# Kernel optimization log

Measured on AMD Instinct MI355X. Metric: run time of the kernel, lower is better.

## Reference

```python
import jax, jax.numpy as jnp
import numpy as np

D = 768      # hidden_size
H = 12       # num_head
HD = D // H  # head_dim
LN_EPS = 1e-5


def setup_inputs() -> dict:
    key = jax.random.key(0)
    ks = jax.random.split(key, 9)
    N, S = 4, 2048
    s = 0.02
    return {
        "hidden_state": jax.random.normal(ks[0], (N, S, D), dtype=jnp.float32),
        "key_padding_mask": jax.random.randint(ks[1], (N, S), 0, 2, dtype=jnp.int64),
        "Wq": jax.random.normal(ks[2], (D, D), dtype=jnp.float32) * s,
        "Wk": jax.random.normal(ks[3], (D, D), dtype=jnp.float32) * s,
        "Wv": jax.random.normal(ks[4], (D, D), dtype=jnp.float32) * s,
        "Wo": jax.random.normal(ks[5], (D, D), dtype=jnp.float32) * s,
        "W1": jax.random.normal(ks[6], (4 * D, D), dtype=jnp.float32) * s,
        "W2": jax.random.normal(ks[7], (D, 4 * D), dtype=jnp.float32) * s,
        "ln_g": jnp.ones((D,), dtype=jnp.float32),
        "ln_b": jnp.zeros((D,), dtype=jnp.float32),
    }


def _layernorm(x, g, b):
    mu = jnp.mean(x, axis=-1, keepdims=True)
    var = jnp.mean(jnp.square(x - mu), axis=-1, keepdims=True)
    return (x - mu) * jax.lax.rsqrt(var + LN_EPS) * g + b


def reference(hidden_state, key_padding_mask, Wq, Wk, Wv, Wo, W1, W2, ln_g, ln_b):
    x = hidden_state
    N, S, _ = x.shape
    # Note: original module projects K and V from `query` (self-attention).
    def proj(W):
        return (x @ W.T).reshape(N, S, H, HD).transpose(0, 2, 1, 3)  # [N,H,S,HD]
    Q, K, V = proj(Wq), proj(Wk), proj(Wv)
    scores = jnp.einsum("bhqd,bhkd->bhqk", Q, K)  # [N,H,S,S]
    # int mask: 0 marks padding positions -> masked with -inf
    pad = (key_padding_mask == 0)[:, None, None, :]  # [N,1,1,S]
    scores = jnp.where(pad, -jnp.inf, scores)
    attn = jax.nn.softmax(scores / np.sqrt(HD), axis=-1)
    ctx = jnp.einsum("bhqk,bhkd->bhqd", attn, V)
    ctx = ctx.transpose(0, 2, 1, 3).reshape(N, S, D)
    mha = ctx @ Wo.T
    # residual + LayerNorm (same LN params used twice, as in the original)
    n1 = _layernorm(x + mha, ln_g, ln_b)
    # FFN with exact GELU (torch nn.GELU default)
    f = jax.nn.gelu(n1 @ W1.T, approximate=False) @ W2.T
    return _layernorm(n1 + f, ln_g, ln_b)
```

## Files before the change

kernel.cpp:

```cpp
#include <hip/hip_runtime.h>
#include <math.h>

typedef unsigned short u16;
typedef unsigned int u32;
typedef __bf16 bf16x8 __attribute__((ext_vector_type(8)));
typedef float f32x4 __attribute__((ext_vector_type(4)));
typedef u32 u32x4 __attribute__((ext_vector_type(4)));

#define NB 4
#define SS 2048
#define DD 768
#define HH 12
#define HD 64
#define ROWS (NB*SS)

__device__ __forceinline__ u16 f2bf(float f) {
    union { float f; unsigned u; } v; v.f = f;
    unsigned r = v.u + 0x7fffu + ((v.u >> 16) & 1u);
    return (u16)(r >> 16);
}
__device__ __forceinline__ u32 fas(float f) { union { float f; u32 u; } v; v.f = f; return v.u; }

__device__ __forceinline__ void gl_lds16(const void* g, void* l) {
    __builtin_amdgcn_global_load_lds((__attribute__((address_space(1))) void*)(g),
                                     (__attribute__((address_space(3))) void*)(l),
                                     16, 0, 0);
}

__global__ __launch_bounds__(256) void prep_kernel(
        const float* __restrict__ X, const float* __restrict__ Wq,
        const float* __restrict__ Wk, const float* __restrict__ Wv,
        const float* __restrict__ Wo, const float* __restrict__ W1,
        const float* __restrict__ W2, const int* __restrict__ mask,
        u16* __restrict__ Xb, u16* __restrict__ Wqkvb, u16* __restrict__ Wob,
        u16* __restrict__ W1b, u16* __restrict__ W2b,
        int* __restrict__ cidx, int* __restrict__ cnt) {
    const int blk = blockIdx.x, tid = threadIdx.x;
    const float* src; u16* dst; int idx;
    if (blk < 6144)       { src = X;  dst = Xb;               idx = blk * 1024 + tid * 4; }
    else if (blk < 6720)  { src = Wq; dst = Wqkvb;            idx = (blk - 6144) * 1024 + tid * 4; }
    else if (blk < 7296)  { src = Wk; dst = Wqkvb + DD * DD;  idx = (blk - 6720) * 1024 + tid * 4; }
    else if (blk < 7872)  { src = Wv; dst = Wqkvb + 2*DD*DD;  idx = (blk - 7296) * 1024 + tid * 4; }
    else if (blk < 8448)  { src = Wo; dst = Wob;              idx = (blk - 7872) * 1024 + tid * 4; }
    else if (blk < 10752) { src = W1; dst = W1b;              idx = (blk - 8448) * 1024 + tid * 4; }
    else if (blk < 13056) { src = W2; dst = W2b;              idx = (blk - 10752) * 1024 + tid * 4; }
    else {
        const int b = blk - 13056;
        const int lane = tid & 63, wave = tid >> 6;
        const int base = b * SS + tid * 8;
        int4 m0 = *(const int4*)&mask[base];
        int4 m1 = *(const int4*)&mask[base + 4];
        int v[8] = { m0.x != 0, m0.y != 0, m0.z != 0, m0.w != 0,
                     m1.x != 0, m1.y != 0, m1.z != 0, m1.w != 0 };
        int own = 0;
#pragma unroll
        for (int i = 0; i < 8; ++i) own += v[i];
        int inc = own;
#pragma unroll
        for (int o = 1; o < 64; o <<= 1) {
            int n = __shfl_up(inc, o);
            if (lane >= o) inc += n;
        }
        __shared__ int wsum[4];
        if (lane == 63) wsum[wave] = inc;
        __syncthreads();
        int wbase = 0;
#pragma unroll
        for (int w = 0; w < 4; ++w) wbase += (w < wave) ? wsum[w] : 0;
        int pos = wbase + inc - own;
        int o8[8];
#pragma unroll
        for (int i = 0; i < 8; ++i) { o8[i] = v[i] ? pos : -1; pos += v[i]; }
        *(int4*)&cidx[base]     = make_int4(o8[0], o8[1], o8[2], o8[3]);
        *(int4*)&cidx[base + 4] = make_int4(o8[4], o8[5], o8[6], o8[7]);
        if (tid == 255) cnt[b] = wbase + inc;
        return;
    }
    float4 v = *(const float4*)&src[idx];
    ushort4 o;
    o.x = f2bf(v.x); o.y = f2bf(v.y); o.z = f2bf(v.z); o.w = f2bf(v.w);
    *(ushort4*)&dst[idx] = o;
}

template <int EPI, int BN, int BK>
__global__ __launch_bounds__(256) void gemm_bt(const u16* __restrict__ A,
                                               const u16* __restrict__ B,
                                               int M, int N, int K,
                                               void* __restrict__ out,
                                               const void* __restrict__ aux,
                                               u16* __restrict__ Qb,
                                               u16* __restrict__ Kb,
                                               u16* __restrict__ Vb,
                                               const int* __restrict__ cidx) {
    constexpr int NH = BK / 64;
    __shared__ __align__(16) u16 lA[NH][128 * 64];
    __shared__ __align__(16) u16 lB[NH][BN * 64];
    constexpr int MI = (BN == 128) ? 4 : 2;
    const int tid = threadIdx.x;
    const int lane = tid & 63, wave = tid >> 6;
    const int quad = lane >> 4, lc = lane & 15;
    const int xcd = blockIdx.x & 7, loc = blockIdx.x >> 3;
    const int mb = xcd * 8 + (loc & 7), nb = loc >> 3;
    const int m0 = mb * 128, n0 = nb * BN;
    const int wrow = (BN == 128) ? (wave >> 1) * 64 : wave * 32;
    const int wcol = (BN == 128) ? (wave & 1) * 64 : 0;
    const int swz = lc & 7;

    f32x4 acc[MI][4] = {};

    for (int kb = 0; kb < K; kb += BK) {
        __syncthreads();
#pragma unroll
        for (int h = 0; h < NH; ++h) {
#pragma unroll
            for (int p0 = 0; p0 < 1024; p0 += 256) {
                int p = p0 + tid, row = p >> 3, cl = (p & 7) ^ (row & 7);
                gl_lds16(A + (size_t)(m0 + row) * K + kb + h * 64 + cl * 8,
                         &lA[h][(size_t)(p0 + wave * 64) * 8]);
            }
#pragma unroll
            for (int p0 = 0; p0 < BN * 8; p0 += 256) {
                int p = p0 + tid, row = p >> 3, cl = (p & 7) ^ (row & 7);
                gl_lds16(B + (size_t)(n0 + row) * K + kb + h * 64 + cl * 8,
                         &lB[h][(size_t)(p0 + wave * 64) * 8]);
            }
        }
        __syncthreads();
#pragma unroll
        for (int h = 0; h < NH; ++h)
#pragma unroll
            for (int k2 = 0; k2 < 2; ++k2) {
                bf16x8 af[MI], bfr[4];
#pragma unroll
                for (int t = 0; t < MI; ++t)
                    af[t] = *(const bf16x8*)&lA[h][(wrow + t * 16 + lc) * 64 + ((quad + k2 * 4) ^ swz) * 8];
#pragma unroll
                for (int t = 0; t < 4; ++t)
                    bfr[t] = *(const bf16x8*)&lB[h][(wcol + t * 16 + lc) * 64 + ((quad + k2 * 4) ^ swz) * 8];
#pragma unroll
                for (int mi = 0; mi < MI; ++mi)
#pragma unroll
                    for (int ni = 0; ni < 4; ++ni)
                        acc[mi][ni] = __builtin_amdgcn_mfma_f32_16x16x32_bf16(af[mi], bfr[ni],
                                                                             acc[mi][ni], 0, 0, 0);
            }
    }

#pragma unroll
    for (int mi = 0; mi < MI; ++mi) {
        int csa[4];
        if constexpr (EPI == 0) {
            int mbase = m0 + wrow + mi * 16 + quad * 4;
            int4 cs4 = *(const int4*)&cidx[(mbase >> 11) * SS + (mbase & 2047)];
            csa[0] = cs4.x; csa[1] = cs4.y; csa[2] = cs4.z; csa[3] = cs4.w;
        }
#pragma unroll
        for (int r = 0; r < 4; ++r) {
            int m = m0 + wrow + mi * 16 + quad * 4 + r;
#pragma unroll
            for (int ni = 0; ni < 4; ++ni) {
                int n = n0 + wcol + ni * 16 + lc;
                float v = acc[mi][ni][r];
                if constexpr (EPI == 0) {
                    int b = m >> 11, s = m & 2047;
                    int which = n / DD, rem = n - which * DD;
                    int h = rem >> 6, d = rem & 63;
                    u16* dst = which == 0 ? Qb : (which == 1 ? Kb : Vb);
                    int sidx = which == 0 ? s : csa[r];
                    if (sidx >= 0)
                        dst[((((size_t)b * HH + h) * SS + sidx) << 6) + d] = f2bf(v);
                } else if constexpr (EPI == 1) {
                    float u = v * fmaf(v * v, 0.035677408f, 0.7978845608f);
                    float e = __builtin_amdgcn_exp2f(u * 2.885390082f);
                    float g = v - v * __builtin_amdgcn_rcpf(e + 1.0f);
                    ((u16*)out)[(size_t)m * N + n] = f2bf(g);
                } else if constexpr (EPI == 2) {
                    ((float*)out)[(size_t)m * N + n] =
                        v + ((const float*)aux)[(size_t)m * N + n];
                } else {
                    ((float*)out)[(size_t)m * N + n] =
                        v + (float)(((const __bf16*)aux)[(size_t)m * N + n]);
                }
            }
        }
    }
}

__global__ __launch_bounds__(256) void transpose_v(const u16* __restrict__ V,
                                                   u16* __restrict__ Vt,
                                                   const int* __restrict__ cnt) {
    __shared__ u16 t[32][33];
    int bh = blockIdx.z;
    int c = cnt[bh / HH];
    int cr = (c + 63) & ~63;
    int s0 = blockIdx.x * 32, d0 = blockIdx.y * 32;
    if (s0 >= cr) return;
    const u16* vb = V + (size_t)bh * SS * HD;
    u16* vtb = Vt + (size_t)bh * HD * SS;
    int tx = threadIdx.x & 31, ty = threadIdx.x >> 5;
#pragma unroll
    for (int i = 0; i < 32; i += 8) {
        int s = s0 + ty + i;
        t[ty + i][tx] = (s < c) ? vb[(size_t)s * HD + d0 + tx] : (u16)0;
    }
    __syncthreads();
#pragma unroll
    for (int i = 0; i < 32; i += 8) vtb[(size_t)(d0 + ty + i) * SS + s0 + tx] = t[tx][ty + i];
}

__global__ __launch_bounds__(256, 3) void attn_kernel(const u16* __restrict__ Q,
                                                      const u16* __restrict__ K,
                                                      const u16* __restrict__ Vt,
                                                      const int* __restrict__ cntg,
                                                      u16* __restrict__ Ctx) {
    __shared__ __align__(16) u16 lK[2][4096];
    __shared__ __align__(16) u16 lV[2][4096];
    const int tid = threadIdx.x, lane = tid & 63, wave = tid >> 6;
    const int quad = lane >> 4, lc = lane & 15;
    const int bh = blockIdx.x % (NB * HH);
    const int b = bh / HH, h = bh - b * HH;
    const int q0 = (blockIdx.x / (NB * HH)) * 128;
    const u16* Qg = Q + ((size_t)bh * SS + q0 + wave * 32) * HD;
    const u16* Kg = K + (size_t)bh * SS * HD;
    const u16* Vg = Vt + (size_t)bh * HD * SS;
    const int sw = lc & 7;
    const int cnt = cntg[b];
    const int nt = (cnt + 63) >> 6;

    const int srow = tid >> 3, scl = (tid & 7) ^ (srow & 7);
    const int srow2 = (256 + tid) >> 3, scl2 = (tid & 7) ^ (srow2 & 7);

    auto stage = [&](int bi, int j0) {
        gl_lds16(Kg + (size_t)(j0 + srow) * HD + scl * 8,   &lK[bi][(size_t)(wave * 64) * 8]);
        gl_lds16(Kg + (size_t)(j0 + srow2) * HD + scl2 * 8, &lK[bi][(size_t)(256 + wave * 64) * 8]);
        gl_lds16(Vg + (size_t)srow * SS + j0 + scl * 8,     &lV[bi][(size_t)(wave * 64) * 8]);
        gl_lds16(Vg + (size_t)srow2 * SS + j0 + scl2 * 8,   &lV[bi][(size_t)(256 + wave * 64) * 8]);
    };

    bf16x8 qf[2][2];
#pragma unroll
    for (int mi = 0; mi < 2; ++mi)
#pragma unroll
        for (int k2 = 0; k2 < 2; ++k2)
            qf[mi][k2] = *(const bf16x8*)(Qg + (size_t)(mi * 16 + lc) * HD + k2 * 32 + quad * 8);

    bf16x8 onesf;
#pragma unroll
    for (int i = 0; i < 8; ++i) onesf[i] = (__bf16)1.0f;

    f32x4 oacc[2][4] = {};
    f32x4 lsum[2] = {};

    stage(0, 0);
    for (int t = 0; t < nt; ++t) {
        const int cur = t & 1;
        if (t < nt - 1) {
            stage(cur ^ 1, (t + 1) * 64);
            __builtin_amdgcn_sched_barrier(0);
            asm volatile("s_waitcnt vmcnt(4)" ::: "memory");
        } else {
            __builtin_amdgcn_sched_barrier(0);
            asm volatile("s_waitcnt vmcnt(0)" ::: "memory");
        }
        __builtin_amdgcn_sched_barrier(0);
        __builtin_amdgcn_s_barrier();
        __builtin_amdgcn_sched_barrier(0);

        const u16* bK = &lK[cur][0];
        const u16* bV = &lV[cur][0];

        f32x4 sacc[2][4] = {};
        __builtin_amdgcn_s_setprio(1);
#pragma unroll
        for (int k2 = 0; k2 < 2; ++k2) {
            bf16x8 kf[4];
#pragma unroll
            for (int ni = 0; ni < 4; ++ni)
                kf[ni] = *(const bf16x8*)&bK[(ni * 16 + lc) * 64 + ((quad + k2 * 4) ^ sw) * 8];
#pragma unroll
            for (int ni = 0; ni < 4; ++ni) {
                sacc[0][ni] = __builtin_amdgcn_mfma_f32_16x16x32_bf16(kf[ni], qf[0][k2], sacc[0][ni], 0, 0, 0);
                sacc[1][ni] = __builtin_amdgcn_mfma_f32_16x16x32_bf16(kf[ni], qf[1][k2], sacc[1][ni], 0, 0, 0);
            }
        }
        __builtin_amdgcn_s_setprio(0);

        const int kb_ = cnt - t * 64;
        const bool part = kb_ < 64;
        u32 pa[2][4], pb[2][4];
#pragma unroll
        for (int ni = 0; ni < 4; ++ni) {
#pragma unroll
            for (int mi = 0; mi < 2; ++mi) {
#pragma unroll
                for (int r = 0; r < 4; ++r) {
                    float e = __builtin_amdgcn_exp2f(sacc[mi][ni][r] * 0.180336880f);
                    if (part) e = (ni * 16 + quad * 4 + r < kb_) ? e : 0.0f;
                    sacc[mi][ni][r] = e;
                }
                pa[mi][ni] = __builtin_amdgcn_perm(fas(sacc[mi][ni][1]), fas(sacc[mi][ni][0]), 0x07060302);
                pb[mi][ni] = __builtin_amdgcn_perm(fas(sacc[mi][ni][3]), fas(sacc[mi][ni][2]), 0x07060302);
            }
        }

        bf16x8 pf[2][2];
#pragma unroll
        for (int mi = 0; mi < 2; ++mi)
#pragma unroll
            for (int k2 = 0; k2 < 2; ++k2) {
                u32 xa = pa[mi][2 * k2], ya = pa[mi][2 * k2 + 1];
                u32 xb = pb[mi][2 * k2], yb = pb[mi][2 * k2 + 1];
                asm("v_permlane32_swap_b32 %0, %1" : "+v"(xa), "+v"(ya));
                asm("v_permlane16_swap_b32 %0, %1" : "+v"(xa), "+v"(ya));
                asm("v_permlane32_swap_b32 %0, %1" : "+v"(xb), "+v"(yb));
                asm("v_permlane16_swap_b32 %0, %1" : "+v"(xb), "+v"(yb));
                u32x4 pw = { xa, xb, ya, yb };
                pf[mi][k2] = __builtin_bit_cast(bf16x8, pw);
            }

        __builtin_amdgcn_s_setprio(1);
#pragma unroll
        for (int k2 = 0; k2 < 2; ++k2) {
            lsum[0] = __builtin_amdgcn_mfma_f32_16x16x32_bf16(pf[0][k2], onesf, lsum[0], 0, 0, 0);
            lsum[1] = __builtin_amdgcn_mfma_f32_16x16x32_bf16(pf[1][k2], onesf, lsum[1], 0, 0, 0);
#pragma unroll
            for (int ni = 0; ni < 4; ++ni) {
                bf16x8 vf = *(const bf16x8*)&bV[(ni * 16 + lc) * 64 + ((quad + k2 * 4) ^ sw) * 8];
                oacc[0][ni] = __builtin_amdgcn_mfma_f32_16x16x32_bf16(pf[0][k2], vf, oacc[0][ni], 0, 0, 0);
                oacc[1][ni] = __builtin_amdgcn_mfma_f32_16x16x32_bf16(pf[1][k2], vf, oacc[1][ni], 0, 0, 0);
            }
        }
        __builtin_amdgcn_s_setprio(0);

        __builtin_amdgcn_sched_barrier(0);
        __builtin_amdgcn_s_barrier();
    }

#pragma unroll
    for (int mi = 0; mi < 2; ++mi)
#pragma unroll
        for (int r = 0; r < 4; ++r) {
            float inv = 1.0f / lsum[mi][r];
            int s = q0 + wave * 32 + mi * 16 + quad * 4 + r;
            size_t base = ((size_t)(b * SS + s)) * DD + h * HD;
#pragma unroll
            for (int ni = 0; ni < 4; ++ni)
                Ctx[base + ni * 16 + lc] = f2bf(oacc[mi][ni][r] * inv);
        }
}

__global__ __launch_bounds__(256) void ln_kernel(const float* __restrict__ in,
                                                 const float* __restrict__ g,
                                                 const float* __restrict__ bb,
                                                 u16* __restrict__ out_bf,
                                                 float* __restrict__ out_f) {
    const int row = blockIdx.x, tid = threadIdx.x;
    const float* x = in + (size_t)row * DD;
    float v0 = x[tid], v1 = x[tid + 256], v2 = x[tid + 512];
    float s = v0 + v1 + v2;
    float q = v0 * v0 + v1 * v1 + v2 * v2;
#pragma unroll
    for (int o = 1; o < 64; o <<= 1) {
        s += __shfl_xor(s, o);
        q += __shfl_xor(q, o);
    }
    __shared__ float rs[4], rq[4];
    int wave = tid >> 6;
    if ((tid & 63) == 0) { rs[wave] = s; rq[wave] = q; }
    __syncthreads();
    s = rs[0] + rs[1] + rs[2] + rs[3];
    q = rq[0] + rq[1] + rq[2] + rq[3];
    float mu = s * (1.0f / DD);
    float var = q * (1.0f / DD) - mu * mu;
    float rstd = rsqrtf(var + 1e-5f);
#pragma unroll
    for (int j = 0; j < 3; ++j) {
        int col = tid + j * 256;
        float v = (j == 0 ? v0 : (j == 1 ? v1 : v2));
        float y = (v - mu) * rstd * g[col] + bb[col];
        if (out_bf) out_bf[(size_t)row * DD + col] = f2bf(y);
        if (out_f) out_f[(size_t)row * DD + col] = y;
    }
}

extern "C" void kernel_launch(void* const* d_in, const int* in_sizes, int n_in,
                              void* d_out, int out_size, void* d_ws, size_t ws_size,
                              hipStream_t stream) {
    const float* X    = (const float*)d_in[0];
    const int*   mask = (const int*)d_in[1];
    const float* Wq   = (const float*)d_in[2];
    const float* Wk   = (const float*)d_in[3];
    const float* Wv   = (const float*)d_in[4];
    const float* Wo   = (const float*)d_in[5];
    const float* W1   = (const float*)d_in[6];
    const float* W2   = (const float*)d_in[7];
    const float* ln_g = (const float*)d_in[8];
    const float* ln_b = (const float*)d_in[9];
    float* out = (float*)d_out;

    char* ws = (char*)d_ws;
    size_t off = 0;
    auto alloc = [&](size_t bytes) {
        void* p = ws + off;
        off += (bytes + 255) & ~(size_t)255;
        return p;
    };
    u16*   Xbf   = (u16*)alloc((size_t)ROWS * DD * 2);
    u16*   Wqkvb = (u16*)alloc((size_t)3 * DD * DD * 2);
    u16*   Wob   = (u16*)alloc((size_t)DD * DD * 2);
    u16*   W1b   = (u16*)alloc((size_t)4 * DD * DD * 2);
    u16*   W2b   = (u16*)alloc((size_t)4 * DD * DD * 2);
    int*   cidx  = (int*)alloc((size_t)NB * SS * 4);
    int*   cnt   = (int*)alloc(256);
    u16*   Qb    = (u16*)alloc((size_t)ROWS * DD * 2);
    u16*   Kb    = (u16*)alloc((size_t)ROWS * DD * 2);
    u16*   Vb    = (u16*)alloc((size_t)ROWS * DD * 2);
    u16*   Vtb   = (u16*)alloc((size_t)ROWS * DD * 2);
    float* resid = (float*)alloc((size_t)ROWS * DD * 4);
    u16*   n1b   = (u16*)alloc((size_t)ROWS * DD * 2);
    u16*   Gb    = Qb;
    u16*   Ctxb  = Xbf;
    float* h2    = resid;

    prep_kernel<<<dim3(13056 + NB), dim3(256), 0, stream>>>(
        X, Wq, Wk, Wv, Wo, W1, W2, mask,
        Xbf, Wqkvb, Wob, W1b, W2b, cidx, cnt);

    gemm_bt<0, 128, 64><<<dim3((3 * DD / 128) * (ROWS / 128)), dim3(256), 0, stream>>>(
        Xbf, Wqkvb, ROWS, 3 * DD, DD, nullptr, nullptr, Qb, Kb, Vb, cidx);

    transpose_v<<<dim3(SS / 32, HD / 32, NB * HH), dim3(256), 0, stream>>>(Vb, Vtb, cnt);

    attn_kernel<<<dim3((SS / 128) * (NB * HH)), dim3(256), 0, stream>>>(
        Qb, Kb, Vtb, cnt, Ctxb);

    gemm_bt<2, 64, 128><<<dim3((DD / 64) * (ROWS / 128)), dim3(256), 0, stream>>>(
        Ctxb, Wob, ROWS, DD, DD, resid, X, nullptr, nullptr, nullptr, nullptr);

    ln_kernel<<<dim3(ROWS), dim3(256), 0, stream>>>(resid, ln_g, ln_b, n1b, nullptr);

    gemm_bt<1, 128, 64><<<dim3((4 * DD / 128) * (ROWS / 128)), dim3(256), 0, stream>>>(
        n1b, W1b, ROWS, 4 * DD, DD, Gb, nullptr, nullptr, nullptr, nullptr, nullptr);

    gemm_bt<3, 64, 128><<<dim3((DD / 64) * (ROWS / 128)), dim3(256), 0, stream>>>(
        Gb, W2b, ROWS, DD, 4 * DD, h2, n1b, nullptr, nullptr, nullptr, nullptr);

    ln_kernel<<<dim3(ROWS), dim3(256), 0, stream>>>(h2, ln_g, ln_b, nullptr, out);
}
```

Measured before the change: 333.9 us.

## Use 256-row GEMM tiles with 512 threads and one-wave-per-row LayerNorm

The GEMM template gains a BM parameter. The QKV and FFN1 GEMMs now run 256x128 tiles with 8 waves, so each B tile is loaded once for twice as many rows, and the XCD-aware block mapping is generalised to match. LayerNorm now handles one row per wavefront with 12 values per lane, which removes the shared-memory reduction and the block barrier. In exchange, the larger tiles use more LDS per block and halve the number of blocks in those GEMMs, which may hurt occupancy and load balance.

```diff
diff --git a/kernel.cpp b/kernel.cpp
--- a/kernel.cpp
+++ b/kernel.cpp
@@ -82,26 +82,28 @@
     *(ushort4*)&dst[idx] = o;
 }
 
-template <int EPI, int BN, int BK>
-__global__ __launch_bounds__(256) void gemm_bt(const u16* __restrict__ A,
-                                               const u16* __restrict__ B,
-                                               int M, int N, int K,
-                                               void* __restrict__ out,
-                                               const void* __restrict__ aux,
-                                               u16* __restrict__ Qb,
-                                               u16* __restrict__ Kb,
-                                               u16* __restrict__ Vb,
-                                               const int* __restrict__ cidx) {
+template <int EPI, int BN, int BK, int BM>
+__global__ __launch_bounds__(BM * 2) void gemm_bt(const u16* __restrict__ A,
+                                                  const u16* __restrict__ B,
+                                                  int M, int N, int K,
+                                                  void* __restrict__ out,
+                                                  const void* __restrict__ aux,
+                                                  u16* __restrict__ Qb,
+                                                  u16* __restrict__ Kb,
+                                                  u16* __restrict__ Vb,
+                                                  const int* __restrict__ cidx) {
     constexpr int NH = BK / 64;
-    __shared__ __align__(16) u16 lA[NH][128 * 64];
+    constexpr int NT = BM * 2;
+    constexpr int MPX = (ROWS / BM) / 8;
+    __shared__ __align__(16) u16 lA[NH][BM * 64];
     __shared__ __align__(16) u16 lB[NH][BN * 64];
     constexpr int MI = (BN == 128) ? 4 : 2;
     const int tid = threadIdx.x;
     const int lane = tid & 63, wave = tid >> 6;
     const int quad = lane >> 4, lc = lane & 15;
     const int xcd = blockIdx.x & 7, loc = blockIdx.x >> 3;
-    const int mb = xcd * 8 + (loc & 7), nb = loc >> 3;
-    const int m0 = mb * 128, n0 = nb * BN;
+    const int mb = xcd * MPX + (loc % MPX), nb = loc / MPX;
+    const int m0 = mb * BM, n0 = nb * BN;
     const int wrow = (BN == 128) ? (wave >> 1) * 64 : wave * 32;
     const int wcol = (BN == 128) ? (wave & 1) * 64 : 0;
     const int swz = lc & 7;
@@ -113,13 +115,13 @@
 #pragma unroll
         for (int h = 0; h < NH; ++h) {
 #pragma unroll
-            for (int p0 = 0; p0 < 1024; p0 += 256) {
+            for (int p0 = 0; p0 < BM * 8; p0 += NT) {
                 int p = p0 + tid, row = p >> 3, cl = (p & 7) ^ (row & 7);
                 gl_lds16(A + (size_t)(m0 + row) * K + kb + h * 64 + cl * 8,
                          &lA[h][(size_t)(p0 + wave * 64) * 8]);
             }
 #pragma unroll
-            for (int p0 = 0; p0 < BN * 8; p0 += 256) {
+            for (int p0 = 0; p0 < BN * 8; p0 += NT) {
                 int p = p0 + tid, row = p >> 3, cl = (p & 7) ^ (row & 7);
                 gl_lds16(B + (size_t)(n0 + row) * K + kb + h * 64 + cl * 8,
                          &lB[h][(size_t)(p0 + wave * 64) * 8]);
@@ -354,30 +356,29 @@
                                                  const float* __restrict__ bb,
                                                  u16* __restrict__ out_bf,
                                                  float* __restrict__ out_f) {
-    const int row = blockIdx.x, tid = threadIdx.x;
+    const int row = blockIdx.x * 4 + (threadIdx.x >> 6);
+    const int lane = threadIdx.x & 63;
     const float* x = in + (size_t)row * DD;
-    float v0 = x[tid], v1 = x[tid + 256], v2 = x[tid + 512];
-    float s = v0 + v1 + v2;
-    float q = v0 * v0 + v1 * v1 + v2 * v2;
+    float v[12];
+    float s = 0.0f, q = 0.0f;
+#pragma unroll
+    for (int i = 0; i < 12; ++i) {
+        v[i] = x[i * 64 + lane];
+        s += v[i];
+        q += v[i] * v[i];
+    }
 #pragma unroll
     for (int o = 1; o < 64; o <<= 1) {
         s += __shfl_xor(s, o);
         q += __shfl_xor(q, o);
     }
-    __shared__ float rs[4], rq[4];
-    int wave = tid >> 6;
-    if ((tid & 63) == 0) { rs[wave] = s; rq[wave] = q; }
-    __syncthreads();
-    s = rs[0] + rs[1] + rs[2] + rs[3];
-    q = rq[0] + rq[1] + rq[2] + rq[3];
     float mu = s * (1.0f / DD);
     float var = q * (1.0f / DD) - mu * mu;
     float rstd = rsqrtf(var + 1e-5f);
 #pragma unroll
-    for (int j = 0; j < 3; ++j) {
-        int col = tid + j * 256;
-        float v = (j == 0 ? v0 : (j == 1 ? v1 : v2));
-        float y = (v - mu) * rstd * g[col] + bb[col];
+    for (int i = 0; i < 12; ++i) {
+        int col = i * 64 + lane;
+        float y = (v[i] - mu) * rstd * g[col] + bb[col];
         if (out_bf) out_bf[(size_t)row * DD + col] = f2bf(y);
         if (out_f) out_f[(size_t)row * DD + col] = y;
     }
@@ -426,7 +427,7 @@
         X, Wq, Wk, Wv, Wo, W1, W2, mask,
         Xbf, Wqkvb, Wob, W1b, W2b, cidx, cnt);
 
-    gemm_bt<0, 128, 64><<<dim3((3 * DD / 128) * (ROWS / 128)), dim3(256), 0, stream>>>(
+    gemm_bt<0, 128, 64, 256><<<dim3((3 * DD / 128) * (ROWS / 256)), dim3(512), 0, stream>>>(
         Xbf, Wqkvb, ROWS, 3 * DD, DD, nullptr, nullptr, Qb, Kb, Vb, cidx);
 
     transpose_v<<<dim3(SS / 32, HD / 32, NB * HH), dim3(256), 0, stream>>>(Vb, Vtb, cnt);
@@ -434,16 +435,16 @@
     attn_kernel<<<dim3((SS / 128) * (NB * HH)), dim3(256), 0, stream>>>(
         Qb, Kb, Vtb, cnt, Ctxb);
 
-    gemm_bt<2, 64, 128><<<dim3((DD / 64) * (ROWS / 128)), dim3(256), 0, stream>>>(
+    gemm_bt<2, 64, 128, 128><<<dim3((DD / 64) * (ROWS / 128)), dim3(256), 0, stream>>>(
         Ctxb, Wob, ROWS, DD, DD, resid, X, nullptr, nullptr, nullptr, nullptr);
 
-    ln_kernel<<<dim3(ROWS), dim3(256), 0, stream>>>(resid, ln_g, ln_b, n1b, nullptr);
-
-    gemm_bt<1, 128, 64><<<dim3((4 * DD / 128) * (ROWS / 128)), dim3(256), 0, stream>>>(
+    ln_kernel<<<dim3(ROWS / 4), dim3(256), 0, stream>>>(resid, ln_g, ln_b, n1b, nullptr);
+
+    gemm_bt<1, 128, 64, 256><<<dim3((4 * DD / 128) * (ROWS / 256)), dim3(512), 0, stream>>>(
         n1b, W1b, ROWS, 4 * DD, DD, Gb, nullptr, nullptr, nullptr, nullptr, nullptr);
 
-    gemm_bt<3, 64, 128><<<dim3((DD / 64) * (ROWS / 128)), dim3(256), 0, stream>>>(
+    gemm_bt<3, 64, 128, 128><<<dim3((DD / 64) * (ROWS / 128)), dim3(256), 0, stream>>>(
         Gb, W2b, ROWS, DD, 4 * DD, h2, n1b, nullptr, nullptr, nullptr, nullptr);
 
-    ln_kernel<<<dim3(ROWS), dim3(256), 0, stream>>>(h2, ln_g, ln_b, nullptr, out);
-}
+    ln_kernel<<<dim3(ROWS / 4), dim3(256), 0, stream>>>(h2, ln_g, ln_b, nullptr, out);
+}
```

Measured after the change: 344.7 us. 1.03x slower.
